# Optimization experiments

Hardware: AMD Instinct MI355X
Metric: run time of the kernel (lower is better)

The kernel has to match this reference:

```python
import jax, jax.numpy as jnp
import numpy as np

HEADS = 16
DIM_HEAD = 64
QUERY_DIM = 1024
CONTEXT_DIM = 1024
D_ATTN = HEADS * DIM_HEAD
SCALE = DIM_HEAD ** -0.5


def setup_inputs() -> dict:
    key = jax.random.key(0)
    ks = jax.random.split(key, 7)
    B, N, M = 4, 2048, 1024
    x = jax.random.normal(ks[0], (B, N, QUERY_DIM), dtype=jnp.float32)
    context = jax.random.normal(ks[1], (B, M, CONTEXT_DIM), dtype=jnp.float32)
    # Linear weights stored as [in, out] (no bias for Q/K/V, bias for to_out)
    s = 0.02
    Wq = jax.random.normal(ks[2], (QUERY_DIM, D_ATTN), dtype=jnp.float32) * s
    Wk = jax.random.normal(ks[3], (CONTEXT_DIM, D_ATTN), dtype=jnp.float32) * s
    Wv = jax.random.normal(ks[4], (CONTEXT_DIM, D_ATTN), dtype=jnp.float32) * s
    Wo = jax.random.normal(ks[5], (D_ATTN, QUERY_DIM), dtype=jnp.float32) * s
    bo = jax.random.normal(ks[6], (QUERY_DIM,), dtype=jnp.float32) * s
    return {"x": x, "context": context, "Wq": Wq, "Wk": Wk, "Wv": Wv, "Wo": Wo, "bo": bo}


def reference(x, context, Wq, Wk, Wv, Wo, bo):
    B, N, _ = x.shape
    M = context.shape[1]
    Q = (x @ Wq).reshape(B, N, HEADS, DIM_HEAD)        # b n h d
    K = (context @ Wk).reshape(B, M, HEADS, DIM_HEAD)  # b m h d
    V = (context @ Wv).reshape(B, M, HEADS, DIM_HEAD)
    # scores: b q h m  (matches torch einsum 'bqhd,bhmd->bqhm')
    scores = jnp.einsum('bqhd,bmhd->bqhm', Q, K) * SCALE
    attn = jax.nn.softmax(scores, axis=-1)
    out = jnp.einsum('bqhm,bmhd->bqhd', attn, V)
    out = out.reshape(B, N, D_ATTN)
    return out @ Wo + bo  # dropout p=0.0 -> identity
```

## Files before the change

### kernel.cpp

```cpp
#include <hip/hip_runtime.h>
#include <math.h>


#define HEADS 16
#define DHEAD 64
#define DM    1024
#define BQ    4
#define NQ    2048
#define MK    1024

typedef unsigned short u16;
typedef __attribute__((ext_vector_type(8))) short bf16x8;
typedef __attribute__((ext_vector_type(2))) float f32x2;
typedef __attribute__((ext_vector_type(4))) float f32x4;
typedef __attribute__((ext_vector_type(16))) float f32x16;

__device__ __forceinline__ u16 f2bf(float f) {
  unsigned u = __builtin_bit_cast(unsigned, f);
  u = u + 0x7FFFu + ((u >> 16) & 1u);
  return (u16)(u >> 16);
}

__device__ __forceinline__ unsigned cvtpk(float lo, float hi2) {
  unsigned r;
  asm("v_cvt_pk_bf16_f32 %0, %1, %2" : "=v"(r) : "v"(lo), "v"(hi2));
  return r;
}

__device__ __forceinline__ float max3f(float a, float b, float c) {
  float d;
  asm("v_max3_f32 %0, %1, %2, %3" : "=v"(d) : "v"(a), "v"(b), "v"(c));
  return d;
}

__device__ __forceinline__ float fexp2(float x) {
  float r;
  asm("v_exp_f32 %0, %1" : "=v"(r) : "v"(x));
  return r;
}

__device__ __forceinline__ f32x2 pk_add(f32x2 a, f32x2 b) {
  f32x2 d;
  asm("v_pk_add_f32 %0, %1, %2" : "=v"(d) : "v"(a), "v"(b));
  return d;
}
__device__ __forceinline__ f32x2 pk_mul(f32x2 a, f32x2 b) {
  f32x2 d;
  asm("v_pk_mul_f32 %0, %1, %2" : "=v"(d) : "v"(a), "v"(b));
  return d;
}

__device__ __forceinline__ void gld16(const u16* g, u16* l) {
  __builtin_amdgcn_global_load_lds((const __attribute__((address_space(1))) void*)g,
                                   (__attribute__((address_space(3))) void*)l,
                                   16, 0, 0);
}

__global__ void k_pre(const float* __restrict__ x, const float* __restrict__ ctx,
                      const float* __restrict__ W0, const float* __restrict__ W1,
                      const float* __restrict__ W2, const float* __restrict__ W3,
                      u16* __restrict__ xb, u16* __restrict__ cb,
                      u16* __restrict__ wt) {
  __shared__ float tsh[32][33];
  int blk = blockIdx.x, t = threadIdx.x;
  if (blk < 6144) {
    const float* in; u16* out; int i;
    if (blk < 4096) { in = x;   out = xb; i = blk * 256 + t; }
    else            { in = ctx; out = cb; i = (blk - 4096) * 256 + t; }
    float4 a = ((const float4*)in)[i * 2];
    float4 b = ((const float4*)in)[i * 2 + 1];
    union { u16 h[8]; int4 v; } r;
    r.h[0] = f2bf(a.x); r.h[1] = f2bf(a.y); r.h[2] = f2bf(a.z); r.h[3] = f2bf(a.w);
    r.h[4] = f2bf(b.x); r.h[5] = f2bf(b.y); r.h[6] = f2bf(b.z); r.h[7] = f2bf(b.w);
    ((int4*)out)[i] = r.v;
    return;
  }
  int vb = blk - 6144;
  int z = vb >> 10, rem = vb & 1023;
  int by = rem >> 5, bx = rem & 31;
  const float* W = z == 0 ? W0 : z == 1 ? W1 : z == 2 ? W2 : W3;
  u16* o = wt + (size_t)z * DM * DM;
  int r0 = by * 32, c0 = bx * 32;
  int tx = t & 31, ty = t >> 5;
  for (int i = ty; i < 32; i += 8) tsh[i][tx] = W[(size_t)(r0 + i) * DM + c0 + tx];
  __syncthreads();
  for (int i = ty; i < 32; i += 8) o[(size_t)(c0 + i) * DM + r0 + tx] = f2bf(tsh[tx][i]);
}

#define VM6 asm volatile("s_waitcnt vmcnt(6)" ::: "memory")

#define STAGE_A8(bufi, h, kof) do {                                          \
  gld16(gA + (size_t)(h) * 131072 + (kof), &As8[bufi][(h) * 8192 + w * 512]); \
  gld16(gA + (size_t)(h) * 131072 + 65536 + (kof),                           \
        &As8[bufi][(h) * 8192 + 4096 + w * 512]);                            \
} while (0)

#define STAGE_B8(bufi, h, kof) do {                                          \
  gld16(gB + (size_t)(h) * 131072 + (kof), &Bs8[bufi][(h) * 8192 + w * 512]); \
  gld16(gB + (size_t)(h) * 131072 + 65536 + (kof),                           \
        &Bs8[bufi][(h) * 8192 + 4096 + w * 512]);                            \
} while (0)

#define RD_A8(qm) do { _Pragma("unroll")                                     \
  for (int mi = 0; mi < 4; ++mi) {                                           \
    const u16* pa = &As8[cur][((qm) * 128 + wmo + mi * 16 + lrow) * 64];     \
    af8[mi][0] = *(const bf16x8*)(pa + fo0);                                 \
    af8[mi][1] = *(const bf16x8*)(pa + (fo0 ^ 32));                          \
  } } while (0)

#define RD_B8(qn) do { _Pragma("unroll")                                     \
  for (int ni = 0; ni < 2; ++ni) {                                           \
    const u16* pb = &Bs8[cur][((qn) * 128 + wno + ni * 16 + lrow) * 64];     \
    bf8[ni][0] = *(const bf16x8*)(pb + fo0);                                 \
    bf8[ni][1] = *(const bf16x8*)(pb + (fo0 ^ 32));                          \
  } } while (0)

#define MM16(qm, qn) do {                                                    \
  __builtin_amdgcn_s_setprio(1);                                             \
  _Pragma("unroll")                                                          \
  for (int mi = 0; mi < 4; ++mi)                                             \
    _Pragma("unroll")                                                        \
    for (int ni = 0; ni < 2; ++ni) {                                         \
      acc[qm][qn][mi][ni] = __builtin_amdgcn_mfma_f32_16x16x32_bf16(         \
          af8[mi][0], bf8[ni][0], acc[qm][qn][mi][ni], 0, 0, 0);             \
      acc[qm][qn][mi][ni] = __builtin_amdgcn_mfma_f32_16x16x32_bf16(         \
          af8[mi][1], bf8[ni][1], acc[qm][qn][mi][ni], 0, 0, 0);             \
    }                                                                        \
  __builtin_amdgcn_s_setprio(0);                                             \
} while (0)

#define PH8(RDS, STG, VM, qm, qn) do {                                       \
  RDS;                                                                       \
  __builtin_amdgcn_sched_barrier(0);                                         \
  STG;                                                                       \
  VM;                                                                        \
  __builtin_amdgcn_s_barrier();                                              \
  asm volatile("s_waitcnt lgkmcnt(0)" ::: "memory");                         \
  __builtin_amdgcn_sched_barrier(0);                                         \
  MM16(qm, qn);                                                              \
  __builtin_amdgcn_sched_barrier(0);                                         \
  __builtin_amdgcn_s_barrier();                                              \
} while (0)

__global__ __launch_bounds__(512, 2) void k_gemm_qkv(const u16* __restrict__ xb,
                                                     const u16* __restrict__ cb,
                                                     const u16* __restrict__ wt,
                                                     u16* __restrict__ Qb,
                                                     u16* __restrict__ Kb,
                                                     u16* __restrict__ Vtb) {
  __shared__ u16 As8[2][16384];
  __shared__ u16 Bs8[2][16384];
  int lin = blockIdx.x;
  int swz = (lin & 7) * 32 + (lin >> 3);
  int p = swz >> 2, bx = swz & 3;
  const u16* A; const u16* Bt; u16* obf; int row0, mode;
  float osc;
  if (p < 32)      { A = xb; Bt = wt;           obf = Qb;  row0 = p * 256;        mode = 0; osc = 0.18033688011112042f; }
  else if (p < 48) { A = cb; Bt = wt + 1048576; obf = Kb;  row0 = (p - 32) * 256; mode = 0; osc = 1.0f; }
  else             { A = cb; Bt = wt + 2097152; obf = Vtb; row0 = (p - 48) * 256; mode = 1; osc = 1.0f; }
  int col0 = bx * 256;
  int t = threadIdx.x;
  int w = t >> 6, lane = t & 63, lrow = lane & 15, lgrp = lane >> 4;
  int wmo = (w >> 2) * 64, wno = (w & 3) * 32;
  int fo0 = (lgrp ^ (lrow & 7)) * 8;
  f32x4 acc[2][2][4][2] = {};
  bf16x8 af8[4][2], bf8[2][2];
  int srow = t >> 3, sunit = (t & 7) ^ ((t >> 3) & 7);
  const u16* gA = A  + (size_t)(row0 + srow) * DM + sunit * 8;
  const u16* gB = Bt + (size_t)(col0 + srow) * DM + sunit * 8;

  STAGE_A8(0, 0, 0);
  STAGE_B8(0, 1, 0);
  STAGE_B8(0, 0, 0);
  STAGE_A8(0, 1, 0);
  STAGE_A8(1, 0, 64);
  STAGE_B8(1, 1, 64);
  VM6;
  __syncthreads();

  #pragma unroll 2
  for (int u = 0; u < 16; ++u) {
    int cur = u & 1, nxt = cur ^ 1;
    int k1 = (u >= 15 ? 15 : u + 1) * 64;
    int k2 = (u >= 14 ? 15 : u + 2) * 64;
    PH8({ RD_A8(0); RD_B8(0); }, STAGE_B8(nxt, 0, k1), VM6,     0, 0);
    PH8({ RD_B8(1); },           STAGE_A8(nxt, 1, k1), (void)0, 0, 1);
    PH8({ RD_A8(1); },           STAGE_A8(cur, 0, k2), (void)0, 1, 1);
    PH8({ RD_B8(0); },           STAGE_B8(cur, 1, k2), VM6,     1, 0);
  }

  #pragma unroll
  for (int qm = 0; qm < 2; ++qm)
    #pragma unroll
    for (int qn = 0; qn < 2; ++qn)
      #pragma unroll
      for (int mi = 0; mi < 4; ++mi)
        #pragma unroll
        for (int ni = 0; ni < 2; ++ni)
          #pragma unroll
          for (int j = 0; j < 4; ++j) {
            int gr = row0 + qm * 128 + wmo + mi * 16 + lgrp * 4 + j;
            int gc = col0 + qn * 128 + wno + ni * 16 + lrow;
            float v = acc[qm][qn][mi][ni][j] * osc;
            if (mode == 0) {
              obf[(size_t)gr * DM + gc] = f2bf(v);
            } else {
              int b = gr >> 10, m = gr & 1023;
              obf[((size_t)(b * DM + gc)) * MK + m] = f2bf(v);
            }
          }
}

#define OSTG_A(bufi, h, kof) do {                                            \
  gld16(gA + (size_t)(h) * 131072 + (kof), &As8[bufi][(h) * 8192 + w * 512]); \
  gld16(gA + (size_t)(h) * 131072 + 65536 + (kof),                           \
        &As8[bufi][(h) * 8192 + 4096 + w * 512]);                            \
} while (0)

#define OSTG_B(bufi, h, kof)                                                 \
  gld16(gB + (size_t)(h) * 65536 + (kof), &Bs8[bufi][(h) * 4096 + w * 512])

#define ORD_A(qm) do { _Pragma("unroll")                                     \
  for (int mi = 0; mi < 2; ++mi) {                                           \
    const u16* pa = &As8[cur][((qm) * 128 + wmo + mi * 16 + lrow) * 64];     \
    af[mi][0] = *(const bf16x8*)(pa + fo0);                                  \
    af[mi][1] = *(const bf16x8*)(pa + (fo0 ^ 32));                           \
  } } while (0)

#define ORD_B(qn, dst) do { _Pragma("unroll")                                \
  for (int ni = 0; ni < 2; ++ni) {                                           \
    const u16* pb = &Bs8[cur][((qn) * 64 + wno + ni * 16 + lrow) * 64];      \
    dst[ni][0] = *(const bf16x8*)(pb + fo0);                                 \
    dst[ni][1] = *(const bf16x8*)(pb + (fo0 ^ 32));                          \
  } } while (0)

#define OMM(qm, qn, bfq) do {                                                \
  __builtin_amdgcn_s_setprio(1);                                             \
  _Pragma("unroll")                                                          \
  for (int mi = 0; mi < 2; ++mi)                                             \
    _Pragma("unroll")                                                        \
    for (int ni = 0; ni < 2; ++ni) {                                         \
      acc[qm][qn][mi][ni] = __builtin_amdgcn_mfma_f32_16x16x32_bf16(         \
          af[mi][0], bfq[ni][0], acc[qm][qn][mi][ni], 0, 0, 0);              \
      acc[qm][qn][mi][ni] = __builtin_amdgcn_mfma_f32_16x16x32_bf16(         \
          af[mi][1], bfq[ni][1], acc[qm][qn][mi][ni], 0, 0, 0);              \
    }                                                                        \
  __builtin_amdgcn_s_setprio(0);                                             \
} while (0)

#define OPH(RDS, STG, VM, qm, qn, bfq) do {                                  \
  RDS;                                                                       \
  __builtin_amdgcn_sched_barrier(0);                                         \
  STG;                                                                       \
  VM;                                                                        \
  __builtin_amdgcn_s_barrier();                                              \
  asm volatile("s_waitcnt lgkmcnt(0)" ::: "memory");                         \
  __builtin_amdgcn_sched_barrier(0);                                         \
  OMM(qm, qn, bfq);                                                          \
  __builtin_amdgcn_sched_barrier(0);                                         \
  __builtin_amdgcn_s_barrier();                                              \
} while (0)

__global__ __launch_bounds__(512, 2) void k_gemm_o(const u16* __restrict__ A,
                                                   const u16* __restrict__ Bt,
                                                   float* __restrict__ of32,
                                                   const float* __restrict__ bias) {
  __shared__ u16 As8[2][16384];
  __shared__ u16 Bs8[2][8192];
  int lin = blockIdx.x;
  int swz = (lin & 7) * 32 + (lin >> 3);
  int p = swz >> 3, bx = swz & 7;
  int row0 = p * 256, col0 = bx * 128;
  int t = threadIdx.x;
  int w = t >> 6, lane = t & 63, lrow = lane & 15, lgrp = lane >> 4;
  int wmo = (w >> 1) * 32, wno = (w & 1) * 32;
  int fo0 = (lgrp ^ (lrow & 7)) * 8;
  f32x4 acc[2][2][2][2] = {};
  bf16x8 af[2][2], bfA[2][2], bfB[2][2];
  int srow = t >> 3, sunit = (t & 7) ^ ((t >> 3) & 7);
  const u16* gA = A  + (size_t)(row0 + srow) * DM + sunit * 8;
  const u16* gB = Bt + (size_t)(col0 + srow) * DM + sunit * 8;

  OSTG_A(0, 0, 0);
  OSTG_B(0, 1, 0);
  OSTG_B(0, 0, 0);
  OSTG_A(0, 1, 0);
  OSTG_A(1, 0, 64);
  OSTG_B(1, 1, 64);
  asm volatile("s_waitcnt vmcnt(5)" ::: "memory");
  __syncthreads();

  #pragma unroll 2
  for (int u = 0; u < 16; ++u) {
    int cur = u & 1, nxt = cur ^ 1;
    int k1 = (u >= 15 ? 15 : u + 1) * 64;
    int k2 = (u >= 14 ? 15 : u + 2) * 64;
    OPH({ ORD_A(0); ORD_B(0, bfA); }, OSTG_B(nxt, 0, k1),
        asm volatile("s_waitcnt vmcnt(4)" ::: "memory"), 0, 0, bfA);
    OPH({ ORD_B(1, bfB); },           OSTG_A(nxt, 1, k1), (void)0, 0, 1, bfB);
    OPH({ ORD_A(1); },                OSTG_A(cur, 0, k2), (void)0, 1, 1, bfB);
    OPH({ (void)0; },                 OSTG_B(cur, 1, k2),
        asm volatile("s_waitcnt vmcnt(5)" ::: "memory"), 1, 0, bfA);
  }

  #pragma unroll
  for (int qm = 0; qm < 2; ++qm)
    #pragma unroll
    for (int qn = 0; qn < 2; ++qn)
      #pragma unroll
      for (int mi = 0; mi < 2; ++mi)
        #pragma unroll
        for (int ni = 0; ni < 2; ++ni)
          #pragma unroll
          for (int j = 0; j < 4; ++j) {
            int gr = row0 + qm * 128 + wmo + mi * 16 + lgrp * 4 + j;
            int gc = col0 + qn * 64 + wno + ni * 16 + lrow;
            of32[(size_t)gr * DM + gc] = acc[qm][qn][mi][ni][j] + bias[gc];
          }
}

#define BUILD_PFRAG(sv, base, frag) {                     \
  unsigned a_ = cvtpk(sv[base + 0], sv[base + 1]);        \
  unsigned c_ = cvtpk(sv[base + 2], sv[base + 3]);        \
  unsigned b_ = cvtpk(sv[base + 4], sv[base + 5]);        \
  unsigned d_ = cvtpk(sv[base + 6], sv[base + 7]);        \
  asm("v_permlane32_swap_b32 %0, %1" : "+v"(a_), "+v"(b_)); \
  asm("v_permlane32_swap_b32 %0, %1" : "+v"(c_), "+v"(d_)); \
  union { unsigned w[4]; bf16x8 v; } u_;                  \
  u_.w[0] = a_;  u_.w[1] = c_;                            \
  u_.w[2] = b_;  u_.w[3] = d_;                            \
  frag = u_.v; }

#define PV_CHUNK(sv, base, c, ms) {                                           \
  bf16x8 pf_; BUILD_PFRAG(sv, base, pf_);                                     \
  int mo_ = (ms) * 64 + ((((c) * 16 + hi * 8)) ^ sw);                         \
  bf16x8 vf0_ = *(const bf16x8*)&Vl[cur][ln * 128 + mo_];                     \
  bf16x8 vf1_ = *(const bf16x8*)&Vl[cur][(32 + ln) * 128 + mo_];              \
  __builtin_amdgcn_s_setprio(1);                                              \
  o0 = __builtin_amdgcn_mfma_f32_32x32x16_bf16(vf0_, pf_, o0, 0, 0, 0);       \
  o1 = __builtin_amdgcn_mfma_f32_32x32x16_bf16(vf1_, pf_, o1, 0, 0, 0);       \
  Lacc = __builtin_amdgcn_mfma_f32_32x32x16_bf16(onesf, pf_, Lacc, 0, 0, 0);  \
  __builtin_amdgcn_s_setprio(0); }

__device__ __forceinline__ float max16(const f32x16 &v) {
  float m0 = max3f(v[0], v[1], v[2]);
  float m1 = max3f(v[3], v[4], v[5]);
  float m2 = max3f(v[6], v[7], v[8]);
  float m3 = max3f(v[9], v[10], v[11]);
  float m4 = max3f(v[12], v[13], v[14]);
  float a = max3f(m0, m1, m2);
  float b = max3f(m3, m4, v[15]);
  return fmaxf(a, b);
}

__global__ __launch_bounds__(512) void k_attn(const u16* __restrict__ Q,
                                              const u16* __restrict__ K,
                                              const u16* __restrict__ Vt,
                                              u16* __restrict__ O) {
  __shared__ __align__(16) u16 Kl[2][8192];
  __shared__ __align__(16) u16 Vl[2][8192];
  int wgid = blockIdx.x;
  int bh = (wgid & 7) * 8 + (wgid >> 6);
  int nt = (wgid >> 3) & 7;
  int b = bh >> 4, h = bh & 15;
  int n0 = nt * 256;
  int t = threadIdx.x, w = t >> 6, lane = t & 63;
  int ln = lane & 31, hi = lane >> 5;

  int qrow = n0 + w * 32 + ln;
  const u16* qp = &Q[(((size_t)(b * NQ + qrow)) * HEADS + h) * DHEAD + hi * 8];
  bf16x8 qf0 = *(const bf16x8*)(qp);
  bf16x8 qf1 = *(const bf16x8*)(qp + 16);
  bf16x8 qf2 = *(const bf16x8*)(qp + 32);
  bf16x8 qf3 = *(const bf16x8*)(qp + 48);

  const short one_ = (short)0x3F80;
  bf16x8 onesf = {one_, one_, one_, one_, one_, one_, one_, one_};

  f32x16 o0 = {}, o1 = {}, Lacc = {};
  float M_ = -1e30f;

  int srK = t >> 3, uK = t & 7;
  const u16* kg = &K[(((size_t)(b * MK + srK)) * HEADS + h) * DHEAD + uK * 8];
  int sdK = srK * 64 + ((uK * 8) ^ ((srK & 7) << 3));
  int srV = t >> 4, uV = t & 15;
  const u16* vg = &Vt[((size_t)(b * DM) + h * DHEAD + srV) * MK + uV * 8];
  int sdV = srV * 128 + ((uV * 8) ^ ((srV & 7) << 3));
  int sw = (ln & 7) << 3;

  int4 kv0 = *(const int4*)kg;
  int4 kv1 = *(const int4*)(kg + 65536);
  int4 vv0 = *(const int4*)vg;
  int4 vv1 = *(const int4*)(vg + 32 * MK);
  *(int4*)&Kl[0][sdK] = kv0;  *(int4*)&Kl[0][sdK + 4096] = kv1;
  *(int4*)&Vl[0][sdV] = vv0;  *(int4*)&Vl[0][sdV + 4096] = vv1;
  __syncthreads();

  for (int it = 0; it < 8; ++it) {
    int cur = it & 1;
    if (it < 7) {
      const u16* kn = kg + (size_t)(it + 1) * 131072;
      const u16* vn = vg + (it + 1) * 128;
      kv0 = *(const int4*)kn;  kv1 = *(const int4*)(kn + 65536);
      vv0 = *(const int4*)vn;  vv1 = *(const int4*)(vn + 32 * MK);
    }

    #pragma unroll
    for (int ms = 0; ms < 2; ++ms) {
      f32x16 s0 = {}, s1 = {};
      __builtin_amdgcn_s_setprio(1);
      #pragma unroll
      for (int kd = 0; kd < 4; ++kd) {
        int doff = (kd * 16 + hi * 8) ^ sw;
        bf16x8 kf0 = *(const bf16x8*)&Kl[cur][(ms * 64 + ln) * 64 + doff];
        bf16x8 kf1 = *(const bf16x8*)&Kl[cur][(ms * 64 + 32 + ln) * 64 + doff];
        bf16x8 qk = kd == 0 ? qf0 : kd == 1 ? qf1 : kd == 2 ? qf2 : qf3;
        s0 = __builtin_amdgcn_mfma_f32_32x32x16_bf16(kf0, qk, s0, 0, 0, 0);
        s1 = __builtin_amdgcn_mfma_f32_32x32x16_bf16(kf1, qk, s1, 0, 0, 0);
      }
      __builtin_amdgcn_s_setprio(0);

      float vm = fmaxf(max16(s0), max16(s1));

      if (!__all(vm - M_ <= 1.44269504f)) {
        float vm2 = fmaxf(vm, __shfl_xor(vm, 32));
        float mn = fmaxf(M_, vm2);
        float rc = fexp2(M_ - mn);
        M_ = mn;
        Lacc[0] *= rc;
        f32x2 rc2 = {rc, rc};
        f32x2* o0p = (f32x2*)&o0;
        f32x2* o1p = (f32x2*)&o1;
        #pragma unroll
        for (int i = 0; i < 8; ++i) { o0p[i] = pk_mul(o0p[i], rc2); }
        #pragma unroll
        for (int i = 0; i < 8; ++i) { o1p[i] = pk_mul(o1p[i], rc2); }
      }
      f32x2 nb2 = {-M_, -M_};
      f32x2* s0p = (f32x2*)&s0;
      f32x2* s1p = (f32x2*)&s1;
      #pragma unroll
      for (int i = 0; i < 8; ++i) s0p[i] = pk_add(s0p[i], nb2);
      #pragma unroll
      for (int i = 0; i < 8; ++i) s1p[i] = pk_add(s1p[i], nb2);
      #pragma unroll
      for (int i = 0; i < 16; ++i) s0[i] = fexp2(s0[i]);
      #pragma unroll
      for (int i = 0; i < 16; ++i) s1[i] = fexp2(s1[i]);

      PV_CHUNK(s0, 0, 0, ms);
      PV_CHUNK(s0, 8, 1, ms);
      PV_CHUNK(s1, 0, 2, ms);
      PV_CHUNK(s1, 8, 3, ms);
    }

    if (it < 7) {
      *(int4*)&Kl[cur ^ 1][sdK] = kv0;  *(int4*)&Kl[cur ^ 1][sdK + 4096] = kv1;
      *(int4*)&Vl[cur ^ 1][sdV] = vv0;  *(int4*)&Vl[cur ^ 1][sdV + 4096] = vv1;
    }
    __syncthreads();
  }

  float inv = 1.0f / Lacc[0];
  u16* ob = (u16*)&O[(((size_t)(b * NQ + qrow)) * HEADS + h) * DHEAD];
  #pragma unroll
  for (int g = 0; g < 4; ++g) {
    union { u16 h4[4]; uint2 v; } r0, r1;
    #pragma unroll
    for (int s = 0; s < 4; ++s) {
      r0.h4[s] = f2bf(o0[4 * g + s] * inv);
      r1.h4[s] = f2bf(o1[4 * g + s] * inv);
    }
    *(uint2*)(ob + 8 * g + 4 * hi) = r0.v;
    *(uint2*)(ob + 32 + 8 * g + 4 * hi) = r1.v;
  }
}

extern "C" void kernel_launch(void* const* d_in, const int* in_sizes, int n_in,
                              void* d_out, int out_size, void* d_ws, size_t ws_size,
                              hipStream_t stream) {
  (void)in_sizes; (void)n_in; (void)out_size; (void)ws_size;
  const float* x   = (const float*)d_in[0];
  const float* ctx = (const float*)d_in[1];
  const float* Wq  = (const float*)d_in[2];
  const float* Wk  = (const float*)d_in[3];
  const float* Wv  = (const float*)d_in[4];
  const float* Wo  = (const float*)d_in[5];
  const float* bo  = (const float*)d_in[6];
  float* out = (float*)d_out;
  char* ws = (char*)d_ws;
  const size_t MB = 1u << 20;
  u16* xb  = (u16*)(ws);
  u16* cb  = (u16*)(ws + 16 * MB);
  u16* wt  = (u16*)(ws + 24 * MB);
  u16* Qb  = (u16*)(ws + 32 * MB);
  u16* Kb  = (u16*)(ws + 48 * MB);
  u16* Vtb = (u16*)(ws + 56 * MB);
  u16* Ab  = (u16*)(ws + 64 * MB);

  k_pre<<<10240, 256, 0, stream>>>(x, ctx, Wq, Wk, Wv, Wo, xb, cb, wt);

  k_gemm_qkv<<<256, 512, 0, stream>>>(xb, cb, wt, Qb, Kb, Vtb);

  k_attn<<<512, 512, 0, stream>>>(Qb, Kb, Vtb, Ab);

  k_gemm_o<<<256, 512, 0, stream>>>(Ab, wt + 3145728, out, bo);
}
```

Baseline: 151.8 us.

## Switch QKV GEMM to 256x128 tiles reusing the output-projection pipeline

```diff
diff --git a/kernel.cpp b/kernel.cpp
--- a/kernel.cpp
+++ b/kernel.cpp
@@ -87,130 +87,6 @@
   for (int i = ty; i < 32; i += 8) o[(size_t)(c0 + i) * DM + r0 + tx] = f2bf(tsh[tx][i]);
 }
 
-#define VM6 asm volatile("s_waitcnt vmcnt(6)" ::: "memory")
-
-#define STAGE_A8(bufi, h, kof) do {                                          \
-  gld16(gA + (size_t)(h) * 131072 + (kof), &As8[bufi][(h) * 8192 + w * 512]); \
-  gld16(gA + (size_t)(h) * 131072 + 65536 + (kof),                           \
-        &As8[bufi][(h) * 8192 + 4096 + w * 512]);                            \
-} while (0)
-
-#define STAGE_B8(bufi, h, kof) do {                                          \
-  gld16(gB + (size_t)(h) * 131072 + (kof), &Bs8[bufi][(h) * 8192 + w * 512]); \
-  gld16(gB + (size_t)(h) * 131072 + 65536 + (kof),                           \
-        &Bs8[bufi][(h) * 8192 + 4096 + w * 512]);                            \
-} while (0)
-
-#define RD_A8(qm) do { _Pragma("unroll")                                     \
-  for (int mi = 0; mi < 4; ++mi) {                                           \
-    const u16* pa = &As8[cur][((qm) * 128 + wmo + mi * 16 + lrow) * 64];     \
-    af8[mi][0] = *(const bf16x8*)(pa + fo0);                                 \
-    af8[mi][1] = *(const bf16x8*)(pa + (fo0 ^ 32));                          \
-  } } while (0)
-
-#define RD_B8(qn) do { _Pragma("unroll")                                     \
-  for (int ni = 0; ni < 2; ++ni) {                                           \
-    const u16* pb = &Bs8[cur][((qn) * 128 + wno + ni * 16 + lrow) * 64];     \
-    bf8[ni][0] = *(const bf16x8*)(pb + fo0);                                 \
-    bf8[ni][1] = *(const bf16x8*)(pb + (fo0 ^ 32));                          \
-  } } while (0)
-
-#define MM16(qm, qn) do {                                                    \
-  __builtin_amdgcn_s_setprio(1);                                             \
-  _Pragma("unroll")                                                          \
-  for (int mi = 0; mi < 4; ++mi)                                             \
-    _Pragma("unroll")                                                        \
-    for (int ni = 0; ni < 2; ++ni) {                                         \
-      acc[qm][qn][mi][ni] = __builtin_amdgcn_mfma_f32_16x16x32_bf16(         \
-          af8[mi][0], bf8[ni][0], acc[qm][qn][mi][ni], 0, 0, 0);             \
-      acc[qm][qn][mi][ni] = __builtin_amdgcn_mfma_f32_16x16x32_bf16(         \
-          af8[mi][1], bf8[ni][1], acc[qm][qn][mi][ni], 0, 0, 0);             \
-    }                                                                        \
-  __builtin_amdgcn_s_setprio(0);                                             \
-} while (0)
-
-#define PH8(RDS, STG, VM, qm, qn) do {                                       \
-  RDS;                                                                       \
-  __builtin_amdgcn_sched_barrier(0);                                         \
-  STG;                                                                       \
-  VM;                                                                        \
-  __builtin_amdgcn_s_barrier();                                              \
-  asm volatile("s_waitcnt lgkmcnt(0)" ::: "memory");                         \
-  __builtin_amdgcn_sched_barrier(0);                                         \
-  MM16(qm, qn);                                                              \
-  __builtin_amdgcn_sched_barrier(0);                                         \
-  __builtin_amdgcn_s_barrier();                                              \
-} while (0)
-
-__global__ __launch_bounds__(512, 2) void k_gemm_qkv(const u16* __restrict__ xb,
-                                                     const u16* __restrict__ cb,
-                                                     const u16* __restrict__ wt,
-                                                     u16* __restrict__ Qb,
-                                                     u16* __restrict__ Kb,
-                                                     u16* __restrict__ Vtb) {
-  __shared__ u16 As8[2][16384];
-  __shared__ u16 Bs8[2][16384];
-  int lin = blockIdx.x;
-  int swz = (lin & 7) * 32 + (lin >> 3);
-  int p = swz >> 2, bx = swz & 3;
-  const u16* A; const u16* Bt; u16* obf; int row0, mode;
-  float osc;
-  if (p < 32)      { A = xb; Bt = wt;           obf = Qb;  row0 = p * 256;        mode = 0; osc = 0.18033688011112042f; }
-  else if (p < 48) { A = cb; Bt = wt + 1048576; obf = Kb;  row0 = (p - 32) * 256; mode = 0; osc = 1.0f; }
-  else             { A = cb; Bt = wt + 2097152; obf = Vtb; row0 = (p - 48) * 256; mode = 1; osc = 1.0f; }
-  int col0 = bx * 256;
-  int t = threadIdx.x;
-  int w = t >> 6, lane = t & 63, lrow = lane & 15, lgrp = lane >> 4;
-  int wmo = (w >> 2) * 64, wno = (w & 3) * 32;
-  int fo0 = (lgrp ^ (lrow & 7)) * 8;
-  f32x4 acc[2][2][4][2] = {};
-  bf16x8 af8[4][2], bf8[2][2];
-  int srow = t >> 3, sunit = (t & 7) ^ ((t >> 3) & 7);
-  const u16* gA = A  + (size_t)(row0 + srow) * DM + sunit * 8;
-  const u16* gB = Bt + (size_t)(col0 + srow) * DM + sunit * 8;
-
-  STAGE_A8(0, 0, 0);
-  STAGE_B8(0, 1, 0);
-  STAGE_B8(0, 0, 0);
-  STAGE_A8(0, 1, 0);
-  STAGE_A8(1, 0, 64);
-  STAGE_B8(1, 1, 64);
-  VM6;
-  __syncthreads();
-
-  #pragma unroll 2
-  for (int u = 0; u < 16; ++u) {
-    int cur = u & 1, nxt = cur ^ 1;
-    int k1 = (u >= 15 ? 15 : u + 1) * 64;
-    int k2 = (u >= 14 ? 15 : u + 2) * 64;
-    PH8({ RD_A8(0); RD_B8(0); }, STAGE_B8(nxt, 0, k1), VM6,     0, 0);
-    PH8({ RD_B8(1); },           STAGE_A8(nxt, 1, k1), (void)0, 0, 1);
-    PH8({ RD_A8(1); },           STAGE_A8(cur, 0, k2), (void)0, 1, 1);
-    PH8({ RD_B8(0); },           STAGE_B8(cur, 1, k2), VM6,     1, 0);
-  }
-
-  #pragma unroll
-  for (int qm = 0; qm < 2; ++qm)
-    #pragma unroll
-    for (int qn = 0; qn < 2; ++qn)
-      #pragma unroll
-      for (int mi = 0; mi < 4; ++mi)
-        #pragma unroll
-        for (int ni = 0; ni < 2; ++ni)
-          #pragma unroll
-          for (int j = 0; j < 4; ++j) {
-            int gr = row0 + qm * 128 + wmo + mi * 16 + lgrp * 4 + j;
-            int gc = col0 + qn * 128 + wno + ni * 16 + lrow;
-            float v = acc[qm][qn][mi][ni][j] * osc;
-            if (mode == 0) {
-              obf[(size_t)gr * DM + gc] = f2bf(v);
-            } else {
-              int b = gr >> 10, m = gr & 1023;
-              obf[((size_t)(b * DM + gc)) * MK + m] = f2bf(v);
-            }
-          }
-}
-
 #define OSTG_A(bufi, h, kof) do {                                            \
   gld16(gA + (size_t)(h) * 131072 + (kof), &As8[bufi][(h) * 8192 + w * 512]); \
   gld16(gA + (size_t)(h) * 131072 + 65536 + (kof),                           \
@@ -260,6 +136,79 @@
   __builtin_amdgcn_sched_barrier(0);                                         \
   __builtin_amdgcn_s_barrier();                                              \
 } while (0)
+
+#define OGEMM_BODY()                                                         \
+  OSTG_A(0, 0, 0);                                                           \
+  OSTG_B(0, 1, 0);                                                           \
+  OSTG_B(0, 0, 0);                                                           \
+  OSTG_A(0, 1, 0);                                                           \
+  OSTG_A(1, 0, 64);                                                          \
+  OSTG_B(1, 1, 64);                                                          \
+  asm volatile("s_waitcnt vmcnt(5)" ::: "memory");                           \
+  __syncthreads();                                                           \
+  _Pragma("unroll 2")                                                        \
+  for (int u = 0; u < 16; ++u) {                                             \
+    int cur = u & 1, nxt = cur ^ 1;                                          \
+    int k1 = (u >= 15 ? 15 : u + 1) * 64;                                    \
+    int k2 = (u >= 14 ? 15 : u + 2) * 64;                                    \
+    OPH({ ORD_A(0); ORD_B(0, bfA); }, OSTG_B(nxt, 0, k1),                    \
+        asm volatile("s_waitcnt vmcnt(4)" ::: "memory"), 0, 0, bfA);         \
+    OPH({ ORD_B(1, bfB); },           OSTG_A(nxt, 1, k1), (void)0, 0, 1, bfB); \
+    OPH({ ORD_A(1); },                OSTG_A(cur, 0, k2), (void)0, 1, 1, bfB); \
+    OPH({ (void)0; },                 OSTG_B(cur, 1, k2),                    \
+        asm volatile("s_waitcnt vmcnt(5)" ::: "memory"), 1, 0, bfA);         \
+  }
+
+__global__ __launch_bounds__(512, 2) void k_gemm_qkv(const u16* __restrict__ xb,
+                                                     const u16* __restrict__ cb,
+                                                     const u16* __restrict__ wt,
+                                                     u16* __restrict__ Qb,
+                                                     u16* __restrict__ Kb,
+                                                     u16* __restrict__ Vtb) {
+  __shared__ u16 As8[2][16384];
+  __shared__ u16 Bs8[2][8192];
+  int lin = blockIdx.x;
+  int swz = (lin & 7) * 64 + (lin >> 3);
+  int p = swz >> 3, bx = swz & 7;
+  const u16* A; const u16* Bt; u16* obf; int row0, mode;
+  float osc;
+  if (p < 32)      { A = xb; Bt = wt;           obf = Qb;  row0 = p * 256;        mode = 0; osc = 0.18033688011112042f; }
+  else if (p < 48) { A = cb; Bt = wt + 1048576; obf = Kb;  row0 = (p - 32) * 256; mode = 0; osc = 1.0f; }
+  else             { A = cb; Bt = wt + 2097152; obf = Vtb; row0 = (p - 48) * 256; mode = 1; osc = 1.0f; }
+  int col0 = bx * 128;
+  int t = threadIdx.x;
+  int w = t >> 6, lane = t & 63, lrow = lane & 15, lgrp = lane >> 4;
+  int wmo = (w >> 1) * 32, wno = (w & 1) * 32;
+  int fo0 = (lgrp ^ (lrow & 7)) * 8;
+  f32x4 acc[2][2][2][2] = {};
+  bf16x8 af[2][2], bfA[2][2], bfB[2][2];
+  int srow = t >> 3, sunit = (t & 7) ^ ((t >> 3) & 7);
+  const u16* gA = A  + (size_t)(row0 + srow) * DM + sunit * 8;
+  const u16* gB = Bt + (size_t)(col0 + srow) * DM + sunit * 8;
+
+  OGEMM_BODY();
+
+  #pragma unroll
+  for (int qm = 0; qm < 2; ++qm)
+    #pragma unroll
+    for (int qn = 0; qn < 2; ++qn)
+      #pragma unroll
+      for (int mi = 0; mi < 2; ++mi)
+        #pragma unroll
+        for (int ni = 0; ni < 2; ++ni)
+          #pragma unroll
+          for (int j = 0; j < 4; ++j) {
+            int gr = row0 + qm * 128 + wmo + mi * 16 + lgrp * 4 + j;
+            int gc = col0 + qn * 64 + wno + ni * 16 + lrow;
+            float v = acc[qm][qn][mi][ni][j] * osc;
+            if (mode == 0) {
+              obf[(size_t)gr * DM + gc] = f2bf(v);
+            } else {
+              int b = gr >> 10, m = gr & 1023;
+              obf[((size_t)(b * DM + gc)) * MK + m] = f2bf(v);
+            }
+          }
+}
 
 __global__ __launch_bounds__(512, 2) void k_gemm_o(const u16* __restrict__ A,
                                                    const u16* __restrict__ Bt,
@@ -281,27 +230,7 @@
   const u16* gA = A  + (size_t)(row0 + srow) * DM + sunit * 8;
   const u16* gB = Bt + (size_t)(col0 + srow) * DM + sunit * 8;
 
-  OSTG_A(0, 0, 0);
-  OSTG_B(0, 1, 0);
-  OSTG_B(0, 0, 0);
-  OSTG_A(0, 1, 0);
-  OSTG_A(1, 0, 64);
-  OSTG_B(1, 1, 64);
-  asm volatile("s_waitcnt vmcnt(5)" ::: "memory");
-  __syncthreads();
-
-  #pragma unroll 2
-  for (int u = 0; u < 16; ++u) {
-    int cur = u & 1, nxt = cur ^ 1;
-    int k1 = (u >= 15 ? 15 : u + 1) * 64;
-    int k2 = (u >= 14 ? 15 : u + 2) * 64;
-    OPH({ ORD_A(0); ORD_B(0, bfA); }, OSTG_B(nxt, 0, k1),
-        asm volatile("s_waitcnt vmcnt(4)" ::: "memory"), 0, 0, bfA);
-    OPH({ ORD_B(1, bfB); },           OSTG_A(nxt, 1, k1), (void)0, 0, 1, bfB);
-    OPH({ ORD_A(1); },                OSTG_A(cur, 0, k2), (void)0, 1, 1, bfB);
-    OPH({ (void)0; },                 OSTG_B(cur, 1, k2),
-        asm volatile("s_waitcnt vmcnt(5)" ::: "memory"), 1, 0, bfA);
-  }
+  OGEMM_BODY();
 
   #pragma unroll
   for (int qm = 0; qm < 2; ++qm)
@@ -500,7 +429,7 @@
 
   k_pre<<<10240, 256, 0, stream>>>(x, ctx, Wq, Wk, Wv, Wo, xb, cb, wt);
 
-  k_gemm_qkv<<<256, 512, 0, stream>>>(xb, cb, wt, Qb, Kb, Vtb);
+  k_gemm_qkv<<<512, 512, 0, stream>>>(xb, cb, wt, Qb, Kb, Vtb);
 
   k_attn<<<512, 512, 0, stream>>>(Qb, Kb, Vtb, Ab);
 
```

Result: slower. 161.2 us (+6.2%).
